# Kernel tuning notes

Measured on AMD Instinct MI355X. Metric: run time of the kernel, lower is better.

## Reference

```python
import jax, jax.numpy as jnp
import numpy as np

BS, DIM, N, M, O = 2048, 32, 40, 40, 200


def setup_inputs() -> dict:
    key = jax.random.key(0)
    k1, k2, k3 = jax.random.split(key, 3)
    x = jax.random.normal(k1, (BS, DIM, N), dtype=jnp.float32)
    y = jax.random.normal(k2, (BS, DIM, M), dtype=jnp.float32)
    # Linear(n*m -> o), no bias; scale like nn.Linear default-ish init
    W = jax.random.normal(k3, (O, N * M), dtype=jnp.float32) * (1.0 / np.sqrt(N * M))
    return {"x": x, "y": y, "W": W}


def reference(x, y, W):
    # Original math: z[b,d,n,m] = x[b,d,n] * y[b,d,m]; flatten (n,m) -> k; out = z @ W.T
    # Fused form: out[b,d,o] = sum_{n,m} x[b,d,n] * y[b,d,m] * W[o, n*M+m]
    o, nm = W.shape
    Wr = W.reshape(o, x.shape[-1], y.shape[-1])  # [O, N, M]
    return jnp.einsum('bdn,bdm,onm->bdo', x, y, Wr)
```

## Files before the change

kernel.cpp:

```cpp
#include <hip/hip_runtime.h>
#include <hip/hip_fp16.h>

#define OOv   200
#define KKv   1600
#define OPAD  208
#define NSTEPS 50
#define NSUPER 25
#define CHUNK_BYTES 13312
#define SUPER_BYTES 26624
#define XSTR 40
#define YSTR 56

typedef _Float16 half8  __attribute__((ext_vector_type(8)));
typedef _Float16 half2v __attribute__((ext_vector_type(2)));
typedef __attribute__((ext_vector_type(4))) float floatx4;

__global__ void wb_convert_kernel(const float* __restrict__ W,
                                  unsigned short* __restrict__ Wh) {
    int idx = blockIdx.x * 256 + threadIdx.x;
    if (idx >= NSTEPS * OPAD * 32) return;
    int j    = idx & 7;
    int slot = (idx >> 3) % (OPAD * 4);
    int c    = (idx >> 3) / (OPAD * 4);
    int o    = slot >> 2;
    int kgs  = slot & 3;
    int kg   = kgs ^ ((o >> 1) & 3);
    int k    = c * 32 + kg * 8 + j;
    float v  = (o < OOv) ? W[o * KKv + k] : 0.0f;
    union { _Float16 h; unsigned short u; } cv; cv.h = (_Float16)v;
    Wh[idx] = cv.u;
}

__global__ __launch_bounds__(256, 2) void cin_mfma_kernel(
        const float* __restrict__ X, const float* __restrict__ Y,
        const unsigned short* __restrict__ Wh, float* __restrict__ Out) {
    __shared__ __align__(16) unsigned char bsm[2 * SUPER_BYTES];
    __shared__ __align__(16) _Float16 xlds[128 * XSTR];
    __shared__ __align__(16) _Float16 ylds[128 * YSTR];

    const int tid     = threadIdx.x;
    const int wave    = tid >> 6;
    const int lane    = tid & 63;
    const int li      = lane & 15;
    const int kg      = lane >> 4;
    const int rowhalf = wave & 1;
    const int colgrp  = wave >> 1;
    const int ntiles  = colgrp ? 6 : 7;
    const int obase   = colgrp * 112;
    const long blockbase = (long)blockIdx.x * 128;

    const float* xg = X + blockbase * 40;
    const float* yg = Y + blockbase * 40;
    for (int i = tid; i < 1280; i += 256) {
        int r  = i / 10;
        int c4 = (i % 10) * 4;
        floatx4 vx = *(const floatx4*)(xg + i * 4);
        floatx4 vy = *(const floatx4*)(yg + i * 4);
        union { half2v h[2]; unsigned long long u; } px, py;
        px.h[0] = (half2v){(_Float16)vx.x, (_Float16)vx.y};
        px.h[1] = (half2v){(_Float16)vx.z, (_Float16)vx.w};
        py.h[0] = (half2v){(_Float16)vy.x, (_Float16)vy.y};
        py.h[1] = (half2v){(_Float16)vy.z, (_Float16)vy.w};
        *(unsigned long long*)(xlds + r * XSTR + c4) = px.u;
        *(unsigned long long*)(ylds + r * YSTR + c4) = py.u;
    }
    {
        const char* src = (const char*)Wh;
        for (int c = wave; c < 26; c += 4) {
            int off = c * 1024 + lane * 16;
            __builtin_amdgcn_global_load_lds(
                (const __attribute__((address_space(1))) unsigned int*)(src + off),
                (__attribute__((address_space(3))) unsigned int*)(bsm + off),
                16, 0, 0);
        }
    }
    __syncthreads();

    floatx4 acc[4][7];
#pragma unroll
    for (int rt = 0; rt < 4; ++rt)
#pragma unroll
        for (int ct = 0; ct < 7; ++ct)
            acc[rt][ct] = (floatx4){0.f, 0.f, 0.f, 0.f};

    const int rowb = rowhalf * 64 + li;
    const char* ybase[4];
    const char* xbase[4];
#pragma unroll
    for (int rt = 0; rt < 4; ++rt) {
        int row = rowb + rt * 16;
        ybase[rt] = (const char*)ylds + row * (YSTR * 2) + kg * 16;
        xbase[rt] = (const char*)xlds + row * (XSTR * 2);
    }
    const bool w1 = kg >= 1, w2 = kg >= 2, w3 = kg >= 3;

    const int bfoff = (obase + li) * 64 + ((kg ^ ((li >> 1) & 3)) * 16);

    const int R32[5] = {0, 64, 48, 32, 16};
    const int B5[5]  = {0, 0, 1, 2, 3};
    const int WK[5]  = {0, 1, 2, 3, 0};

    for (int g = 0; g < 5; ++g) {
        half2v xd[4][8];
#pragma unroll
        for (int rt = 0; rt < 4; ++rt) {
            half8 xq = *(const half8*)(xbase[rt] + g * 16);
#pragma unroll
            for (int e = 0; e < 8; ++e)
                xd[rt][e] = (half2v){xq[e], xq[e]};
        }

#pragma unroll
        for (int ss = 0; ss < 5; ++ss) {
            const int sstep = g * 5 + ss;
            if (sstep + 1 < NSUPER) {
                const char* src = (const char*)Wh + (size_t)(sstep + 1) * SUPER_BYTES;
                unsigned char* dst = bsm + ((sstep + 1) & 1) * SUPER_BYTES;
                for (int c = wave; c < 26; c += 4) {
                    int off = c * 1024 + lane * 16;
                    __builtin_amdgcn_global_load_lds(
                        (const __attribute__((address_space(1))) unsigned int*)(src + off),
                        (__attribute__((address_space(3))) unsigned int*)(dst + off),
                        16, 0, 0);
                }
            }
            const unsigned char* cbuf = bsm + (sstep & 1) * SUPER_BYTES;

#pragma unroll
            for (int half = 0; half < 2; ++half) {
                const int p  = 2 * ss + half;
                const int pm = p % 5, pd = p / 5;
                const int yimm  = R32[pm];
                const int dbase = B5[pm] + 4 * pd;
                const int wk    = WK[pm];
                const bool use  = (wk == 1) ? w1 : (wk == 2) ? w2 : (wk == 3) ? w3 : false;
                const unsigned char* chunk = cbuf + half * CHUNK_BYTES;

                half8 bf[7];
#pragma unroll
                for (int ct = 0; ct < 7; ++ct)
                    if (ct < ntiles)
                        bf[ct] = *(const half8*)(chunk + bfoff + ct * 1024);

                half8 af[4];
#pragma unroll
                for (int rt = 0; rt < 4; ++rt) {
                    const char* ya = ybase[rt] + (yimm - (use ? 80 : 0));
                    half8 yv = *(const half8*)ya;
                    half2v xs = use ? xd[rt][dbase + 1] : xd[rt][dbase];
                    half8 xsp = __builtin_shufflevector(xs, xs, 0, 1, 0, 1, 0, 1, 0, 1);
                    af[rt] = xsp * yv;
                }

#pragma unroll
                for (int ct = 0; ct < 7; ++ct)
                    if (ct < ntiles)
#pragma unroll
                        for (int rt = 0; rt < 4; ++rt)
                            acc[rt][ct] = __builtin_amdgcn_mfma_f32_16x16x32_f16(
                                af[rt], bf[ct], acc[rt][ct], 0, 0, 0);
            }
            __syncthreads();
        }
    }

#pragma unroll
    for (int rt = 0; rt < 4; ++rt) {
#pragma unroll
        for (int ct = 0; ct < 7; ++ct) {
            if (ct >= ntiles) continue;
            int gcol = obase + ct * 16 + li;
            if (gcol < OOv) {
#pragma unroll
                for (int r4 = 0; r4 < 4; ++r4) {
                    long grow = blockbase + rowhalf * 64 + rt * 16 + kg * 4 + r4;
                    Out[grow * OOv + gcol] = acc[rt][ct][r4];
                }
            }
        }
    }
}

extern "C" void kernel_launch(void* const* d_in, const int* in_sizes, int n_in,
                              void* d_out, int out_size, void* d_ws, size_t ws_size,
                              hipStream_t stream) {
    (void)in_sizes; (void)n_in; (void)out_size; (void)ws_size;
    const float* X = (const float*)d_in[0];
    const float* Y = (const float*)d_in[1];
    const float* W = (const float*)d_in[2];
    float* Out = (float*)d_out;
    unsigned short* Wh = (unsigned short*)d_ws;

    wb_convert_kernel<<<1300, 256, 0, stream>>>(W, Wh);
    cin_mfma_kernel<<<512, 256, 0, stream>>>(X, Y, Wh, Out);
}
```

Before: 122.1 us.

## Split output columns across two blocks and hold Y fragments in registers

```diff
diff --git a/kernel.cpp b/kernel.cpp
--- a/kernel.cpp
+++ b/kernel.cpp
@@ -7,9 +7,9 @@
 #define NSTEPS 50
 #define NSUPER 25
 #define CHUNK_BYTES 13312
-#define SUPER_BYTES 26624
+#define HALF0_BYTES 7168
 #define XSTR 40
-#define YSTR 56
+#define YSTR 40
 
 typedef _Float16 half8  __attribute__((ext_vector_type(8)));
 typedef _Float16 half2v __attribute__((ext_vector_type(2)));
@@ -21,11 +21,11 @@
     if (idx >= NSTEPS * OPAD * 32) return;
     int j    = idx & 7;
     int slot = (idx >> 3) % (OPAD * 4);
-    int c    = (idx >> 3) / (OPAD * 4);
+    int t    = (idx >> 3) / (OPAD * 4);
     int o    = slot >> 2;
     int kgs  = slot & 3;
     int kg   = kgs ^ ((o >> 1) & 3);
-    int k    = c * 32 + kg * 8 + j;
+    int k    = (4 * (t / 5) + kg) * 40 + 8 * (t % 5) + j;
     float v  = (o < OOv) ? W[o * KKv + k] : 0.0f;
     union { _Float16 h; unsigned short u; } cv; cv.h = (_Float16)v;
     Wh[idx] = cv.u;
@@ -34,7 +34,7 @@
 __global__ __launch_bounds__(256, 2) void cin_mfma_kernel(
         const float* __restrict__ X, const float* __restrict__ Y,
         const unsigned short* __restrict__ Wh, float* __restrict__ Out) {
-    __shared__ __align__(16) unsigned char bsm[2 * SUPER_BYTES];
+    __shared__ __align__(16) unsigned char bsm[2 * HALF0_BYTES * 2];
     __shared__ __align__(16) _Float16 xlds[128 * XSTR];
     __shared__ __align__(16) _Float16 ylds[128 * YSTR];
 
@@ -45,9 +45,14 @@
     const int kg      = lane >> 4;
     const int rowhalf = wave & 1;
     const int colgrp  = wave >> 1;
-    const int ntiles  = colgrp ? 6 : 7;
-    const int obase   = colgrp * 112;
-    const long blockbase = (long)blockIdx.x * 128;
+
+    const int ch      = blockIdx.x & 1;
+    const long blockbase = (long)(blockIdx.x >> 1) * 128;
+    const int htiles  = ch ? 6 : 7;
+    const int ntiles  = colgrp ? htiles - 4 : 4;
+    const int nt      = ch ? (colgrp ? 3 : 3) : (colgrp ? 3 : 4);
+    const int cbt     = ch ? (colgrp ? 3 : 0) : (colgrp ? 4 : 0);
+    const int half_bytes = ch ? 6144 : 7168;
 
     const float* xg = X + blockbase * 40;
     const float* yg = Y + blockbase * 40;
@@ -65,96 +70,97 @@
         *(unsigned long long*)(ylds + r * YSTR + c4) = py.u;
     }
     {
-        const char* src = (const char*)Wh;
-        for (int c = wave; c < 26; c += 4) {
-            int off = c * 1024 + lane * 16;
-            __builtin_amdgcn_global_load_lds(
-                (const __attribute__((address_space(1))) unsigned int*)(src + off),
-                (__attribute__((address_space(3))) unsigned int*)(bsm + off),
-                16, 0, 0);
-        }
-    }
-    __syncthreads();
-
-    floatx4 acc[4][7];
-#pragma unroll
-    for (int rt = 0; rt < 4; ++rt)
-#pragma unroll
-        for (int ct = 0; ct < 7; ++ct)
-            acc[rt][ct] = (floatx4){0.f, 0.f, 0.f, 0.f};
-
-    const int rowb = rowhalf * 64 + li;
-    const char* ybase[4];
-    const char* xbase[4];
-#pragma unroll
-    for (int rt = 0; rt < 4; ++rt) {
-        int row = rowb + rt * 16;
-        ybase[rt] = (const char*)ylds + row * (YSTR * 2) + kg * 16;
-        xbase[rt] = (const char*)xlds + row * (XSTR * 2);
-    }
-    const bool w1 = kg >= 1, w2 = kg >= 2, w3 = kg >= 3;
-
-    const int bfoff = (obase + li) * 64 + ((kg ^ ((li >> 1) & 3)) * 16);
-
-    const int R32[5] = {0, 64, 48, 32, 16};
-    const int B5[5]  = {0, 0, 1, 2, 3};
-    const int WK[5]  = {0, 1, 2, 3, 0};
-
-    for (int g = 0; g < 5; ++g) {
-        half2v xd[4][8];
-#pragma unroll
-        for (int rt = 0; rt < 4; ++rt) {
-            half8 xq = *(const half8*)(xbase[rt] + g * 16);
-#pragma unroll
-            for (int e = 0; e < 8; ++e)
-                xd[rt][e] = (half2v){xq[e], xq[e]};
-        }
-
-#pragma unroll
-        for (int ss = 0; ss < 5; ++ss) {
-            const int sstep = g * 5 + ss;
-            if (sstep + 1 < NSUPER) {
-                const char* src = (const char*)Wh + (size_t)(sstep + 1) * SUPER_BYTES;
-                unsigned char* dst = bsm + ((sstep + 1) & 1) * SUPER_BYTES;
-                for (int c = wave; c < 26; c += 4) {
-                    int off = c * 1024 + lane * 16;
+        const char* src0 = (const char*)Wh + ch * HALF0_BYTES;
+        for (int q = 0; q < 2; ++q) {
+            const char* src = src0 + (size_t)q * CHUNK_BYTES;
+            unsigned char* dst = bsm + q * HALF0_BYTES;
+            for (int u = wave; u * 1024 < half_bytes; u += 4) {
+                int off = u * 1024 + lane * 16;
+                if (off < half_bytes)
                     __builtin_amdgcn_global_load_lds(
                         (const __attribute__((address_space(1))) unsigned int*)(src + off),
                         (__attribute__((address_space(3))) unsigned int*)(dst + off),
                         16, 0, 0);
+            }
+        }
+    }
+    __syncthreads();
+
+    const int rowb = rowhalf * 64 + li;
+    half8 yr[4][5];
+#pragma unroll
+    for (int rt = 0; rt < 4; ++rt) {
+        int row = rowb + rt * 16;
+#pragma unroll
+        for (int grp = 0; grp < 5; ++grp)
+            yr[rt][grp] = *(const half8*)(ylds + row * YSTR + grp * 8);
+    }
+
+    floatx4 acc[4][4];
+#pragma unroll
+    for (int rt = 0; rt < 4; ++rt)
+#pragma unroll
+        for (int ct = 0; ct < 4; ++ct)
+            acc[rt][ct] = (floatx4){0.f, 0.f, 0.f, 0.f};
+
+    const int lc0   = cbt * 16 + li;
+    const int bfoff = lc0 * 64 + ((kg ^ ((lc0 >> 1) & 3)) * 16);
+
+    for (int mg = 0; mg < 5; ++mg) {
+        half2v xs[2][4];
+#pragma unroll
+        for (int w = 0; w < 2; ++w)
+#pragma unroll
+            for (int rt = 0; rt < 4; ++rt) {
+                _Float16 xv = xlds[(rowb + rt * 16) * XSTR + (2 * mg + w) * 4 + kg];
+                xs[w][rt] = (half2v){xv, xv};
+            }
+
+#pragma unroll
+        for (int ss5 = 0; ss5 < 5; ++ss5) {
+            const int sstep = mg * 5 + ss5;
+            if (sstep + 1 < NSUPER) {
+                const char* src0 = (const char*)Wh + ch * HALF0_BYTES
+                                 + (size_t)(2 * sstep + 2) * CHUNK_BYTES;
+                unsigned char* dst0 = bsm + ((sstep + 1) & 1) * (2 * HALF0_BYTES);
+                for (int q = 0; q < 2; ++q)
+                    for (int u = wave; u * 1024 < half_bytes; u += 4) {
+                        int off = u * 1024 + lane * 16;
+                        if (off < half_bytes)
+                            __builtin_amdgcn_global_load_lds(
+                                (const __attribute__((address_space(1))) unsigned int*)
+                                    (src0 + (size_t)q * CHUNK_BYTES + off),
+                                (__attribute__((address_space(3))) unsigned int*)
+                                    (dst0 + q * HALF0_BYTES + off),
+                                16, 0, 0);
+                    }
+            }
+            const unsigned char* cbuf = bsm + (sstep & 1) * (2 * HALF0_BYTES);
+
+#pragma unroll
+            for (int h = 0; h < 2; ++h) {
+                const int t  = 2 * sstep + h;
+                const int p  = t % 5;
+                const int w  = (t / 5) & 1;
+                const unsigned char* chunk = cbuf + h * HALF0_BYTES;
+
+                half8 bf[4];
+#pragma unroll
+                for (int ct = 0; ct < 4; ++ct)
+                    if (ct < nt)
+                        bf[ct] = *(const half8*)(chunk + bfoff + ct * 1024);
+
+                half8 af[4];
+#pragma unroll
+                for (int rt = 0; rt < 4; ++rt) {
+                    half8 xsp = __builtin_shufflevector(xs[w][rt], xs[w][rt],
+                                                        0, 1, 0, 1, 0, 1, 0, 1);
+                    af[rt] = xsp * yr[rt][p];
                 }
-            }
-            const unsigned char* cbuf = bsm + (sstep & 1) * SUPER_BYTES;
-
-#pragma unroll
-            for (int half = 0; half < 2; ++half) {
-                const int p  = 2 * ss + half;
-                const int pm = p % 5, pd = p / 5;
-                const int yimm  = R32[pm];
-                const int dbase = B5[pm] + 4 * pd;
-                const int wk    = WK[pm];
-                const bool use  = (wk == 1) ? w1 : (wk == 2) ? w2 : (wk == 3) ? w3 : false;
-                const unsigned char* chunk = cbuf + half * CHUNK_BYTES;
-
-                half8 bf[7];
-#pragma unroll
-                for (int ct = 0; ct < 7; ++ct)
-                    if (ct < ntiles)
-                        bf[ct] = *(const half8*)(chunk + bfoff + ct * 1024);
-
-                half8 af[4];
-#pragma unroll
-                for (int rt = 0; rt < 4; ++rt) {
-                    const char* ya = ybase[rt] + (yimm - (use ? 80 : 0));
-                    half8 yv = *(const half8*)ya;
-                    half2v xs = use ? xd[rt][dbase + 1] : xd[rt][dbase];
-                    half8 xsp = __builtin_shufflevector(xs, xs, 0, 1, 0, 1, 0, 1, 0, 1);
-                    af[rt] = xsp * yv;
-                }
-
-#pragma unroll
-                for (int ct = 0; ct < 7; ++ct)
-                    if (ct < ntiles)
+
+#pragma unroll
+                for (int ct = 0; ct < 4; ++ct)
+                    if (ct < nt)
 #pragma unroll
                         for (int rt = 0; rt < 4; ++rt)
                             acc[rt][ct] = __builtin_amdgcn_mfma_f32_16x16x32_f16(
@@ -167,9 +173,9 @@
 #pragma unroll
     for (int rt = 0; rt < 4; ++rt) {
 #pragma unroll
-        for (int ct = 0; ct < 7; ++ct) {
-            if (ct >= ntiles) continue;
-            int gcol = obase + ct * 16 + li;
+        for (int ct = 0; ct < 4; ++ct) {
+            if (ct >= nt) continue;
+            int gcol = ch * 112 + (cbt + ct) * 16 + li;
             if (gcol < OOv) {
 #pragma unroll
                 for (int r4 = 0; r4 < 4; ++r4) {
@@ -192,5 +198,5 @@
     unsigned short* Wh = (unsigned short*)d_ws;
 
     wb_convert_kernel<<<1300, 256, 0, stream>>>(W, Wh);
-    cin_mfma_kernel<<<512, 256, 0, stream>>>(X, Y, Wh, Out);
+    cin_mfma_kernel<<<1024, 256, 0, stream>>>(X, Y, Wh, Out);
 }
```

Measured after the change: 136.5 us. 1.12x slower.
